# Kernel tuning notes

Hardware: AMD Instinct MI355X
Metric: run time of the kernel (lower is better)

Reference implementation:

```python
import jax, jax.numpy as jnp
import numpy as np

INIT_RANGE = 1e-4


def setup_inputs() -> dict:
    key = jax.random.key(0)
    k1, k2, k3, k4 = jax.random.split(key, 4)
    n, m = 2048, 2048
    K, p, q, r = 64, 32, 32, 1
    weights = jax.random.normal(k1, (n, m), dtype=jnp.float32)
    # uniform(-init_range, init_range) as in nn.init.uniform_
    pos_weights = jax.random.uniform(k2, (K, n // p, m // q), dtype=jnp.float32,
                                     minval=-INIT_RANGE, maxval=INIT_RANGE)
    # LowRankMatrix factors for the (K, p, q) prototypes
    proto_w = jax.random.normal(k3, (K, p, r), dtype=jnp.float32)
    proto_h = jax.random.normal(k4, (K, r, q), dtype=jnp.float32)
    return {"weights": weights, "pos_weights": pos_weights,
            "proto_w": proto_w, "proto_h": proto_h}


def reference(weights, pos_weights, proto_w, proto_h):
    # prototypes: (K, p, q) from low-rank factors
    protos = jnp.einsum('kpr,krq->kpq', proto_w, proto_h)
    K, I, J = pos_weights.shape          # I = n/p, J = m/q
    p, q = protos.shape[1], protos.shape[2]
    # sum_k kron(pos_weights[k], protos[k]):
    # delta[i*p+a, j*q+b] = sum_k pos[k,i,j] * proto[k,a,b]
    delta = jnp.einsum('kij,kab->iajb', pos_weights, protos).reshape(I * p, J * q)
    return weights + delta
```

## Files before the change

kernel.cpp:

```cpp
#include <hip/hip_runtime.h>


#define KDIM 64

__global__ __launch_bounds__(256) void splopa_kernel(
    const float* __restrict__ weights,
    const float* __restrict__ pos,
    const float* __restrict__ pw,
    const float* __restrict__ ph,
    float* __restrict__ out)
{
    __shared__ float w_lds[KDIM * 32];
    __shared__ float h_lds[KDIM * 32];

    const int tid = threadIdx.x;

    {
        const float4* wg = (const float4*)pw;
        const float4* hg = (const float4*)ph;
        float4* wl = (float4*)w_lds;
        float4* hl = (float4*)h_lds;
        wl[tid]       = wg[tid];
        wl[tid + 256] = wg[tid + 256];
        hl[tid]       = hg[tid];
        hl[tid + 256] = hg[tid + 256];
    }

    const int wave = tid >> 6;
    const int lane = tid & 63;

    const int t = (blockIdx.x << 2) + wave;
    const int i = t >> 6;
    const int j = t & 63;
    int ij = (i << 6) + j;
    ij = __builtin_amdgcn_readfirstlane(ij);

    const int a0 = (lane >> 3) << 2;
    const int b0 = (lane & 7) << 2;

    const int row0 = (i << 5) + a0;
    const int col0 = (j << 5) + b0;
    const float* wptr = weights + (size_t)row0 * 2048 + col0;
    float*       optr = out     + (size_t)row0 * 2048 + col0;

    float4 wt0 = *(const float4*)(wptr);
    float4 wt1 = *(const float4*)(wptr + 2048);
    float4 wt2 = *(const float4*)(wptr + 4096);
    float4 wt3 = *(const float4*)(wptr + 6144);

    float4 acc0 = {0.f, 0.f, 0.f, 0.f};
    float4 acc1 = {0.f, 0.f, 0.f, 0.f};
    float4 acc2 = {0.f, 0.f, 0.f, 0.f};
    float4 acc3 = {0.f, 0.f, 0.f, 0.f};

    __syncthreads();

    #pragma unroll
    for (int k = 0; k < KDIM; ++k) {
        const float  pk = pos[(k << 12) + ij];
        const float4 wv = *(const float4*)&w_lds[(k << 5) + a0];
        const float4 hv = *(const float4*)&h_lds[(k << 5) + b0];

        const float t0 = pk * wv.x;
        const float t1 = pk * wv.y;
        const float t2 = pk * wv.z;
        const float t3 = pk * wv.w;

        acc0.x += t0 * hv.x; acc0.y += t0 * hv.y; acc0.z += t0 * hv.z; acc0.w += t0 * hv.w;
        acc1.x += t1 * hv.x; acc1.y += t1 * hv.y; acc1.z += t1 * hv.z; acc1.w += t1 * hv.w;
        acc2.x += t2 * hv.x; acc2.y += t2 * hv.y; acc2.z += t2 * hv.z; acc2.w += t2 * hv.w;
        acc3.x += t3 * hv.x; acc3.y += t3 * hv.y; acc3.z += t3 * hv.z; acc3.w += t3 * hv.w;
    }

    wt0.x += acc0.x; wt0.y += acc0.y; wt0.z += acc0.z; wt0.w += acc0.w;
    wt1.x += acc1.x; wt1.y += acc1.y; wt1.z += acc1.z; wt1.w += acc1.w;
    wt2.x += acc2.x; wt2.y += acc2.y; wt2.z += acc2.z; wt2.w += acc2.w;
    wt3.x += acc3.x; wt3.y += acc3.y; wt3.z += acc3.z; wt3.w += acc3.w;

    *(float4*)(optr)        = wt0;
    *(float4*)(optr + 2048) = wt1;
    *(float4*)(optr + 4096) = wt2;
    *(float4*)(optr + 6144) = wt3;
}

extern "C" void kernel_launch(void* const* d_in, const int* in_sizes, int n_in,
                              void* d_out, int out_size, void* d_ws, size_t ws_size,
                              hipStream_t stream) {
    const float* weights = (const float*)d_in[0];
    const float* pos     = (const float*)d_in[1];
    const float* pw      = (const float*)d_in[2];
    const float* ph      = (const float*)d_in[3];
    float* out = (float*)d_out;

    splopa_kernel<<<1024, 256, 0, stream>>>(weights, pos, pw, ph, out);
}
```

Measured before the change: 81.78 us.

## Process two blocks per wave and broadcast pos weights via readlane

Each wave now computes two adjacent 32x32 output blocks, reusing the LDS prototype loads across both. The 64 per-block pos coefficients are loaded once with one vectorized load per lane and broadcast with readlane in the loop, replacing 64 scalar global loads. The grid is halved to 512 blocks and all weight loads are issued before the LDS fill. This adds register pressure from 32 accumulators plus 32 held weight values, and halving the block count reduces the parallelism available for latency hiding.

```diff
diff --git a/kernel.cpp b/kernel.cpp
--- a/kernel.cpp
+++ b/kernel.cpp
@@ -13,7 +13,34 @@
     __shared__ float w_lds[KDIM * 32];
     __shared__ float h_lds[KDIM * 32];
 
-    const int tid = threadIdx.x;
+    const int tid  = threadIdx.x;
+    const int wave = tid >> 6;
+    const int lane = tid & 63;
+
+    const int tp = (blockIdx.x << 2) + wave;
+    const int i  = tp >> 5;
+    const int j0 = (tp & 31) << 1;
+    int ij = (i << 6) + j0;
+    ij = __builtin_amdgcn_readfirstlane(ij);
+
+    const float2 vpk = *(const float2*)&pos[((size_t)lane << 12) + ij];
+
+    const int a0 = (lane >> 3) << 2;
+    const int b0 = (lane & 7) << 2;
+
+    const int row0 = (i << 5) + a0;
+    const int col0 = (j0 << 5) + b0;
+    const float* wptr = weights + (size_t)row0 * 2048 + col0;
+    float*       optr = out     + (size_t)row0 * 2048 + col0;
+
+    float4 wt00 = *(const float4*)(wptr);
+    float4 wt01 = *(const float4*)(wptr + 2048);
+    float4 wt02 = *(const float4*)(wptr + 4096);
+    float4 wt03 = *(const float4*)(wptr + 6144);
+    float4 wt10 = *(const float4*)(wptr + 32);
+    float4 wt11 = *(const float4*)(wptr + 2048 + 32);
+    float4 wt12 = *(const float4*)(wptr + 4096 + 32);
+    float4 wt13 = *(const float4*)(wptr + 6144 + 32);
 
     {
         const float4* wg = (const float4*)pw;
@@ -26,61 +53,50 @@
         hl[tid + 256] = hg[tid + 256];
     }
 
-    const int wave = tid >> 6;
-    const int lane = tid & 63;
-
-    const int t = (blockIdx.x << 2) + wave;
-    const int i = t >> 6;
-    const int j = t & 63;
-    int ij = (i << 6) + j;
-    ij = __builtin_amdgcn_readfirstlane(ij);
-
-    const int a0 = (lane >> 3) << 2;
-    const int b0 = (lane & 7) << 2;
-
-    const int row0 = (i << 5) + a0;
-    const int col0 = (j << 5) + b0;
-    const float* wptr = weights + (size_t)row0 * 2048 + col0;
-    float*       optr = out     + (size_t)row0 * 2048 + col0;
-
-    float4 wt0 = *(const float4*)(wptr);
-    float4 wt1 = *(const float4*)(wptr + 2048);
-    float4 wt2 = *(const float4*)(wptr + 4096);
-    float4 wt3 = *(const float4*)(wptr + 6144);
-
-    float4 acc0 = {0.f, 0.f, 0.f, 0.f};
-    float4 acc1 = {0.f, 0.f, 0.f, 0.f};
-    float4 acc2 = {0.f, 0.f, 0.f, 0.f};
-    float4 acc3 = {0.f, 0.f, 0.f, 0.f};
+    float4 a00 = {0.f,0.f,0.f,0.f}, a01 = {0.f,0.f,0.f,0.f};
+    float4 a02 = {0.f,0.f,0.f,0.f}, a03 = {0.f,0.f,0.f,0.f};
+    float4 a10 = {0.f,0.f,0.f,0.f}, a11 = {0.f,0.f,0.f,0.f};
+    float4 a12 = {0.f,0.f,0.f,0.f}, a13 = {0.f,0.f,0.f,0.f};
 
     __syncthreads();
 
     #pragma unroll
     for (int k = 0; k < KDIM; ++k) {
-        const float  pk = pos[(k << 12) + ij];
         const float4 wv = *(const float4*)&w_lds[(k << 5) + a0];
         const float4 hv = *(const float4*)&h_lds[(k << 5) + b0];
+        const float pk0 = __uint_as_float(
+            __builtin_amdgcn_readlane(__float_as_uint(vpk.x), k));
+        const float pk1 = __uint_as_float(
+            __builtin_amdgcn_readlane(__float_as_uint(vpk.y), k));
 
-        const float t0 = pk * wv.x;
-        const float t1 = pk * wv.y;
-        const float t2 = pk * wv.z;
-        const float t3 = pk * wv.w;
-
-        acc0.x += t0 * hv.x; acc0.y += t0 * hv.y; acc0.z += t0 * hv.z; acc0.w += t0 * hv.w;
-        acc1.x += t1 * hv.x; acc1.y += t1 * hv.y; acc1.z += t1 * hv.z; acc1.w += t1 * hv.w;
-        acc2.x += t2 * hv.x; acc2.y += t2 * hv.y; acc2.z += t2 * hv.z; acc2.w += t2 * hv.w;
-        acc3.x += t3 * hv.x; acc3.y += t3 * hv.y; acc3.z += t3 * hv.z; acc3.w += t3 * hv.w;
+        float t;
+        t = pk0 * wv.x; a00.x += t*hv.x; a00.y += t*hv.y; a00.z += t*hv.z; a00.w += t*hv.w;
+        t = pk0 * wv.y; a01.x += t*hv.x; a01.y += t*hv.y; a01.z += t*hv.z; a01.w += t*hv.w;
+        t = pk0 * wv.z; a02.x += t*hv.x; a02.y += t*hv.y; a02.z += t*hv.z; a02.w += t*hv.w;
+        t = pk0 * wv.w; a03.x += t*hv.x; a03.y += t*hv.y; a03.z += t*hv.z; a03.w += t*hv.w;
+        t = pk1 * wv.x; a10.x += t*hv.x; a10.y += t*hv.y; a10.z += t*hv.z; a10.w += t*hv.w;
+        t = pk1 * wv.y; a11.x += t*hv.x; a11.y += t*hv.y; a11.z += t*hv.z; a11.w += t*hv.w;
+        t = pk1 * wv.z; a12.x += t*hv.x; a12.y += t*hv.y; a12.z += t*hv.z; a12.w += t*hv.w;
+        t = pk1 * wv.w; a13.x += t*hv.x; a13.y += t*hv.y; a13.z += t*hv.z; a13.w += t*hv.w;
     }
 
-    wt0.x += acc0.x; wt0.y += acc0.y; wt0.z += acc0.z; wt0.w += acc0.w;
-    wt1.x += acc1.x; wt1.y += acc1.y; wt1.z += acc1.z; wt1.w += acc1.w;
-    wt2.x += acc2.x; wt2.y += acc2.y; wt2.z += acc2.z; wt2.w += acc2.w;
-    wt3.x += acc3.x; wt3.y += acc3.y; wt3.z += acc3.z; wt3.w += acc3.w;
+    wt00.x += a00.x; wt00.y += a00.y; wt00.z += a00.z; wt00.w += a00.w;
+    wt01.x += a01.x; wt01.y += a01.y; wt01.z += a01.z; wt01.w += a01.w;
+    wt02.x += a02.x; wt02.y += a02.y; wt02.z += a02.z; wt02.w += a02.w;
+    wt03.x += a03.x; wt03.y += a03.y; wt03.z += a03.z; wt03.w += a03.w;
+    wt10.x += a10.x; wt10.y += a10.y; wt10.z += a10.z; wt10.w += a10.w;
+    wt11.x += a11.x; wt11.y += a11.y; wt11.z += a11.z; wt11.w += a11.w;
+    wt12.x += a12.x; wt12.y += a12.y; wt12.z += a12.z; wt12.w += a12.w;
+    wt13.x += a13.x; wt13.y += a13.y; wt13.z += a13.z; wt13.w += a13.w;
 
-    *(float4*)(optr)        = wt0;
-    *(float4*)(optr + 2048) = wt1;
-    *(float4*)(optr + 4096) = wt2;
-    *(float4*)(optr + 6144) = wt3;
+    *(float4*)(optr)             = wt00;
+    *(float4*)(optr + 2048)      = wt01;
+    *(float4*)(optr + 4096)      = wt02;
+    *(float4*)(optr + 6144)      = wt03;
+    *(float4*)(optr + 32)        = wt10;
+    *(float4*)(optr + 2048 + 32) = wt11;
+    *(float4*)(optr + 4096 + 32) = wt12;
+    *(float4*)(optr + 6144 + 32) = wt13;
 }
 
 extern "C" void kernel_launch(void* const* d_in, const int* in_sizes, int n_in,
@@ -92,5 +108,5 @@
     const float* ph      = (const float*)d_in[3];
     float* out = (float*)d_out;
 
-    splopa_kernel<<<1024, 256, 0, stream>>>(weights, pos, pw, ph, out);
+    splopa_kernel<<<512, 256, 0, stream>>>(weights, pos, pw, ph, out);
 }
```

New measurement: 80.56 us. About the same (-1.5%).
